# Kernel optimization log

Hardware: AMD Instinct MI355X
Metric: run time of the kernel (lower is better)

Reference implementation:

```python
import jax, jax.numpy as jnp
import numpy as np

TOP_K = 8  # num_experts_per_tok


def setup_inputs() -> dict:
    key = jax.random.key(0)
    ks = jax.random.split(key, 5)
    B, S, H = 2, 2048, 1024
    E, F = 16, 2816
    return {
        "hidden_states": jax.random.normal(ks[0], (B, S, H), dtype=jnp.float32),
        "router_w": jax.random.normal(ks[1], (E, H), dtype=jnp.float32) * (1.0 / np.sqrt(H)),
        "gate_w": jax.random.normal(ks[2], (E, F, H), dtype=jnp.float32) * (1.0 / np.sqrt(H)),
        "up_w": jax.random.normal(ks[3], (E, F, H), dtype=jnp.float32) * (1.0 / np.sqrt(H)),
        "down_w": jax.random.normal(ks[4], (E, H, F), dtype=jnp.float32) * (1.0 / np.sqrt(F)),
    }


def reference(hidden_states, router_w, gate_w, up_w, down_w):
    B, S, H = hidden_states.shape
    E = router_w.shape[0]
    x = hidden_states.reshape(-1, H)            # [T, H]
    T = x.shape[0]

    # Router: top-k expert selection, softmax over selected logits.
    logits = x @ router_w.T                      # [T, E]
    topk_vals, topk_idx = jax.lax.top_k(logits, TOP_K)
    topk_w = jax.nn.softmax(topk_vals, axis=-1)  # [T, K], sums to 1 -> no renorm needed

    # Dense combine weights [T, E] (scatter top-k weights per token).
    dense_w = jnp.zeros((T, E), dtype=x.dtype).at[
        jnp.arange(T)[:, None], topk_idx
    ].add(topk_w)

    # SwiGLU expert MLPs, batched over all experts (dense MoE reference).
    g = jnp.einsum('th,efh->etf', x, gate_w)     # [E, T, F]
    u = jnp.einsum('th,efh->etf', x, up_w)       # [E, T, F]
    h = jax.nn.silu(g) * u                       # [E, T, F]
    out_e = jnp.einsum('etf,ehf->eth', h, down_w)  # [E, T, H]

    out = jnp.einsum('te,eth->th', dense_w, out_e)  # weighted combine
    return out.reshape(B, S, H)
```

## Files before the change

kernel.cpp:

```cpp
#include <hip/hip_runtime.h>
#include <hip/hip_bf16.h>
#include <stdint.h>
#include <math.h>

#define T_TOK 4096
#define HD    1024
#define NE    16
#define FF    2816
#define TOPK  8
#define NPAIR (T_TOK*TOPK)

typedef __attribute__((ext_vector_type(8))) __bf16 bf16x8;
typedef __attribute__((ext_vector_type(4))) float  f32x4;

__device__ __forceinline__ unsigned short f2bf(float x){
  union { float f; unsigned u; } c; c.f = x;
  unsigned r = (c.u + 0x7FFFu + ((c.u >> 16) & 1u)) >> 16;
  return (unsigned short)r;
}
__device__ __forceinline__ float bf2f(unsigned short h){
  union { unsigned u; float f; } c; c.u = ((unsigned)h) << 16; return c.f;
}

__device__ __forceinline__ void gload16(const void* src, void* lds_dst){
  __builtin_amdgcn_global_load_lds((const __attribute__((address_space(1))) unsigned int*)src,
                                   (__attribute__((address_space(3))) unsigned int*)lds_dst,
                                   16, 0, 0);
}

__global__ __launch_bounds__(256) void convert3_kernel(
    const float* __restrict__ g, const float* __restrict__ u, const float* __restrict__ d,
    unsigned short* __restrict__ gb, unsigned short* __restrict__ ub, unsigned short* __restrict__ db,
    int n4each)
{
  int i = blockIdx.x * blockDim.x + threadIdx.x;
  int stride = gridDim.x * blockDim.x;
  int total = 3 * n4each;
  for (; i < total; i += stride){
    const float* s; unsigned short* dst; int j;
    if (i < n4each){ s = g; dst = gb; j = i; }
    else if (i < 2*n4each){ s = u; dst = ub; j = i - n4each; }
    else { s = d; dst = db; j = i - 2*n4each; }
    float4 v = ((const float4*)s)[j];
    ushort4 o;
    o.x = f2bf(v.x); o.y = f2bf(v.y); o.z = f2bf(v.z); o.w = f2bf(v.w);
    ((ushort4*)dst)[j] = o;
  }
}

__global__ __launch_bounds__(256) void router_kernel(
    const float* __restrict__ x, const float* __restrict__ rw,
    unsigned short* __restrict__ xbf, int* __restrict__ topk_idx, float* __restrict__ topk_w)
{
  __shared__ float xs[HD];
  __shared__ float lg[NE];
  const int t   = blockIdx.x;
  const int tid = threadIdx.x;
  const int lane = tid & 63;
  const int wid  = tid >> 6;

  float4 v = ((const float4*)(x + (size_t)t*HD))[tid];
  ((float4*)xs)[tid] = v;
  ushort4 o;
  o.x = f2bf(v.x); o.y = f2bf(v.y); o.z = f2bf(v.z); o.w = f2bf(v.w);
  ((ushort4*)(xbf + (size_t)t*HD))[tid] = o;
  __syncthreads();

  for (int ee = 0; ee < 4; ++ee){
    int e = wid*4 + ee;
    const float* w = rw + (size_t)e*HD;
    float p = 0.f;
    for (int j = lane; j < HD; j += 64) p += xs[j] * w[j];
    #pragma unroll
    for (int offs = 32; offs; offs >>= 1) p += __shfl_xor(p, offs, 64);
    if (lane == 0) lg[e] = p;
  }
  __syncthreads();

  if (tid == 0){
    float vals[NE];
    #pragma unroll
    for (int e = 0; e < NE; ++e) vals[e] = lg[e];
    int   idx[TOPK]; float tv[TOPK];
    for (int k = 0; k < TOPK; ++k){
      int bi = 0; float bv = -3.4e38f;
      for (int e = 0; e < NE; ++e) if (vals[e] > bv){ bv = vals[e]; bi = e; }
      idx[k] = bi; tv[k] = bv; vals[bi] = -3.4e38f;
    }
    float m = tv[0];
    float ex[TOPK]; float s = 0.f;
    for (int k = 0; k < TOPK; ++k){ ex[k] = expf(tv[k] - m); s += ex[k]; }
    float inv = 1.f / s;
    for (int k = 0; k < TOPK; ++k){
      topk_idx[t*TOPK + k] = idx[k];
      topk_w [t*TOPK + k] = ex[k] * inv;
    }
  }
}

__global__ __launch_bounds__(256) void lists_kernel(
    const int* __restrict__ topk_idx,
    int* __restrict__ rows, int* __restrict__ slot_of,
    int* __restrict__ cnt, int* __restrict__ offs_out)
{
  const int e = blockIdx.x;
  const int tid = threadIdx.x;
  const int lane = tid & 63;
  const int wid  = tid >> 6;

  __shared__ int wred[4];
  __shared__ int wred2[4];
  __shared__ int soff;

  int nlt = 0, ceq = 0;
  for (int t = tid; t < T_TOK; t += 256){
    #pragma unroll
    for (int k = 0; k < TOPK; ++k){
      int vv = topk_idx[t*TOPK + k];
      nlt += (vv < e) ? 1 : 0;
      ceq += (vv == e) ? 1 : 0;
    }
  }
  #pragma unroll
  for (int offs = 32; offs; offs >>= 1){
    nlt += __shfl_xor(nlt, offs, 64);
    ceq += __shfl_xor(ceq, offs, 64);
  }
  if (lane == 0){ wred[wid] = nlt; wred2[wid] = ceq; }
  __syncthreads();
  if (tid == 0){
    int off = wred[0] + wred[1] + wred[2] + wred[3];
    int c   = wred2[0] + wred2[1] + wred2[2] + wred2[3];
    offs_out[e] = off;
    cnt[e] = c;
    soff = off;
  }
  __syncthreads();
  const int off = soff;

  __shared__ int wc[4];
  int base = 0;
  for (int c0 = 0; c0 < T_TOK; c0 += 256){
    int t = c0 + tid;
    int kpos = -1;
    #pragma unroll
    for (int k = 0; k < TOPK; ++k) if (topk_idx[t*TOPK + k] == e) kpos = k;
    bool f = (kpos >= 0);
    unsigned long long m = __ballot(f);
    if (lane == 0) wc[wid] = __popcll(m);
    __syncthreads();
    int p = base;
    for (int w = 0; w < wid; ++w) p += wc[w];
    p += __popcll(m & ((1ULL << lane) - 1ULL));
    if (f){
      rows[off + p] = t;
      slot_of[t*TOPK + kpos] = off + p;
    }
    int tot = wc[0] + wc[1] + wc[2] + wc[3];
    __syncthreads();
    base += tot;
  }
}

__global__ __launch_bounds__(256, 3) void gemm_gateup(
    const unsigned short* __restrict__ xbf,
    const unsigned short* __restrict__ gw,
    const unsigned short* __restrict__ uw,
    const int* __restrict__ rows, const int* __restrict__ cnt, const int* __restrict__ offs,
    unsigned short* __restrict__ hbuf)
{
  const int cpx = gridDim.x >> 3;
  const int bid = blockIdx.x;
  const int nid = (bid & 7) * cpx + (bid >> 3);
  const int mb   = nid & 31;
  const int rest = nid >> 5;
  const int nb   = rest % (FF/64);
  const int e    = rest / (FF/64);

  const int c  = cnt[e];
  const int m0 = mb * 128;
  if (m0 >= c) return;
  const int n0 = nb * 64;
  const int off_e = offs[e];

  __shared__ unsigned short As[128*64];
  __shared__ unsigned short Bg[64*64];
  __shared__ unsigned short Bu[64*64];

  const int tid  = threadIdx.x;
  const int lane = tid & 63;
  const int wid  = tid >> 6;
  const int ar = lane & 15;
  const int kb = lane >> 4;
  const int wm = wid >> 1;
  const int wn = wid & 1;

  const unsigned short* asrc[4];
  #pragma unroll
  for (int j = 0; j < 4; ++j){
    int cj = j*256 + tid;
    int r  = cj >> 3;
    int sw = ((cj & 7) ^ (r & 7)) * 8;
    int rm = m0 + r; if (rm > c-1) rm = c-1;
    asrc[j] = xbf + (size_t)rows[off_e + rm]*HD + sw;
  }
  const unsigned short* bgsrc[2];
  const unsigned short* busrc[2];
  #pragma unroll
  for (int j = 0; j < 2; ++j){
    int cj = j*256 + tid;
    int r  = cj >> 3;
    int sw = ((cj & 7) ^ (r & 7)) * 8;
    bgsrc[j] = gw + ((size_t)e*FF + n0 + r)*HD + sw;
    busrc[j] = uw + ((size_t)e*FF + n0 + r)*HD + sw;
  }

  f32x4 accg[4][2] = {};
  f32x4 accu[4][2] = {};

  for (int ks = 0; ks < HD/64; ++ks){
    #pragma unroll
    for (int j = 0; j < 4; ++j)
      gload16(asrc[j] + ks*64, &As[(j*256+tid)*8]);
    #pragma unroll
    for (int j = 0; j < 2; ++j){
      gload16(bgsrc[j] + ks*64, &Bg[(j*256+tid)*8]);
      gload16(busrc[j] + ks*64, &Bu[(j*256+tid)*8]);
    }
    __syncthreads();
    #pragma unroll
    for (int kk = 0; kk < 2; ++kk){
      bf16x8 a[4], fg[2], fu[2];
      #pragma unroll
      for (int m = 0; m < 4; ++m){
        int r = wm*64 + m*16 + ar;
        a[m] = *(const bf16x8*)&As[r*64 + (((kk*4 + kb) ^ (r & 7))*8)];
      }
      #pragma unroll
      for (int n = 0; n < 2; ++n){
        int rf = wn*32 + n*16 + ar;
        int o  = rf*64 + (((kk*4 + kb) ^ (rf & 7))*8);
        fg[n] = *(const bf16x8*)&Bg[o];
        fu[n] = *(const bf16x8*)&Bu[o];
      }
      #pragma unroll
      for (int m = 0; m < 4; ++m){
        #pragma unroll
        for (int n = 0; n < 2; ++n){
          accg[m][n] = __builtin_amdgcn_mfma_f32_16x16x32_bf16(a[m], fg[n], accg[m][n], 0, 0, 0);
          accu[m][n] = __builtin_amdgcn_mfma_f32_16x16x32_bf16(a[m], fu[n], accu[m][n], 0, 0, 0);
        }
      }
    }
    __syncthreads();
  }

  #pragma unroll
  for (int m = 0; m < 4; ++m){
    #pragma unroll
    for (int n = 0; n < 2; ++n){
      int fcol = n0 + wn*32 + n*16 + ar;
      #pragma unroll
      for (int i = 0; i < 4; ++i){
        int gr = m0 + wm*64 + m*16 + kb*4 + i;
        if (gr < c){
          float g = accg[m][n][i];
          float u = accu[m][n][i];
          float s = g / (1.0f + expf(-g));
          hbuf[(size_t)(off_e + gr)*FF + fcol] = f2bf(s * u);
        }
      }
    }
  }
}

__global__ __launch_bounds__(256, 3) void gemm_down(
    const unsigned short* __restrict__ hbuf,
    const unsigned short* __restrict__ dw,
    const int* __restrict__ cnt, const int* __restrict__ offs,
    unsigned short* __restrict__ ybuf)
{
  const int cpx = gridDim.x >> 3;
  const int bid = blockIdx.x;
  const int nid = (bid & 7) * cpx + (bid >> 3);
  const int mb   = nid & 31;
  const int rest = nid >> 5;
  const int nb   = rest & 7;
  const int e    = rest >> 3;

  const int c  = cnt[e];
  const int m0 = mb * 128;
  if (m0 >= c) return;
  const int n0 = nb * 128;
  const int off_e = offs[e];

  __shared__ unsigned short As[128*64];
  __shared__ unsigned short Bs[128*64];

  const int tid  = threadIdx.x;
  const int lane = tid & 63;
  const int wid  = tid >> 6;
  const int ar = lane & 15;
  const int kb = lane >> 4;
  const int wm = wid >> 1;
  const int wn = wid & 1;

  const unsigned short* asrc[4];
  const unsigned short* bsrc[4];
  #pragma unroll
  for (int j = 0; j < 4; ++j){
    int cj = j*256 + tid;
    int r  = cj >> 3;
    int sw = ((cj & 7) ^ (r & 7)) * 8;
    int rm = m0 + r; if (rm > c-1) rm = c-1;
    asrc[j] = hbuf + (size_t)(off_e + rm)*FF + sw;
    bsrc[j] = dw + ((size_t)e*HD + n0 + r)*FF + sw;
  }

  f32x4 acc[4][4] = {};

  for (int ks = 0; ks < FF/64; ++ks){
    #pragma unroll
    for (int j = 0; j < 4; ++j){
      gload16(asrc[j] + ks*64, &As[(j*256+tid)*8]);
      gload16(bsrc[j] + ks*64, &Bs[(j*256+tid)*8]);
    }
    __syncthreads();
    #pragma unroll
    for (int kk = 0; kk < 2; ++kk){
      bf16x8 a[4], b[4];
      #pragma unroll
      for (int m = 0; m < 4; ++m){
        int r = wm*64 + m*16 + ar;
        a[m] = *(const bf16x8*)&As[r*64 + (((kk*4 + kb) ^ (r & 7))*8)];
      }
      #pragma unroll
      for (int n = 0; n < 4; ++n){
        int r = wn*64 + n*16 + ar;
        b[n] = *(const bf16x8*)&Bs[r*64 + (((kk*4 + kb) ^ (r & 7))*8)];
      }
      #pragma unroll
      for (int m = 0; m < 4; ++m){
        #pragma unroll
        for (int n = 0; n < 4; ++n){
          acc[m][n] = __builtin_amdgcn_mfma_f32_16x16x32_bf16(a[m], b[n], acc[m][n], 0, 0, 0);
        }
      }
    }
    __syncthreads();
  }

  #pragma unroll
  for (int m = 0; m < 4; ++m){
    #pragma unroll
    for (int n = 0; n < 4; ++n){
      int col = n0 + wn*64 + n*16 + ar;
      #pragma unroll
      for (int i = 0; i < 4; ++i){
        int gr = m0 + wm*64 + m*16 + kb*4 + i;
        if (gr < c){
          ybuf[(size_t)(off_e + gr)*HD + col] = f2bf(acc[m][n][i]);
        }
      }
    }
  }
}

__global__ __launch_bounds__(256) void combine_kernel(
    const unsigned short* __restrict__ ybuf,
    const int* __restrict__ slot_of, const float* __restrict__ topk_w,
    float* __restrict__ out)
{
  const int t   = blockIdx.x;
  const int tid = threadIdx.x;
  const int c0  = tid * 4;
  float4 acc = {0.f, 0.f, 0.f, 0.f};
  #pragma unroll
  for (int k = 0; k < TOPK; ++k){
    int slot = slot_of[t*TOPK + k];
    float w  = topk_w[t*TOPK + k];
    ushort4 v = *(const ushort4*)&ybuf[(size_t)slot*HD + c0];
    acc.x += w * bf2f(v.x);
    acc.y += w * bf2f(v.y);
    acc.z += w * bf2f(v.z);
    acc.w += w * bf2f(v.w);
  }
  ((float4*)out)[(size_t)t*(HD/4) + tid] = acc;
}

extern "C" void kernel_launch(void* const* d_in, const int* in_sizes, int n_in,
                              void* d_out, int out_size, void* d_ws, size_t ws_size,
                              hipStream_t stream)
{
  const float* x  = (const float*)d_in[0];
  const float* rw = (const float*)d_in[1];
  const float* gw = (const float*)d_in[2];
  const float* uw = (const float*)d_in[3];
  const float* dw = (const float*)d_in[4];
  float* out = (float*)d_out;

  char* ws = (char*)d_ws;
  size_t off = 0;
  auto alloc = [&](size_t b) -> void* {
    void* p = ws + off;
    off += (b + 255) & ~(size_t)255;
    return p;
  };

  unsigned short* gwb  = (unsigned short*)alloc((size_t)NE*FF*HD*2);
  unsigned short* uwb  = (unsigned short*)alloc((size_t)NE*FF*HD*2);
  unsigned short* dwb  = (unsigned short*)alloc((size_t)NE*HD*FF*2);
  unsigned short* xbf  = (unsigned short*)alloc((size_t)T_TOK*HD*2);
  unsigned short* hbuf = (unsigned short*)alloc((size_t)NPAIR*FF*2);
  unsigned short* ybuf = (unsigned short*)alloc((size_t)NPAIR*HD*2);
  int*   tki   = (int*)alloc((size_t)T_TOK*TOPK*4);
  float* tkw   = (float*)alloc((size_t)T_TOK*TOPK*4);
  int*   rowsb = (int*)alloc((size_t)NPAIR*4);
  int*   slotf = (int*)alloc((size_t)NPAIR*4);
  int*   cntb  = (int*)alloc(NE*4);
  int*   offsb = (int*)alloc(NE*4);

  const int n4 = NE*FF*HD/4;
  convert3_kernel<<<4096, 256, 0, stream>>>(gw, uw, dw, gwb, uwb, dwb, n4);

  router_kernel<<<T_TOK, 256, 0, stream>>>(x, rw, xbf, tki, tkw);
  lists_kernel<<<NE, 256, 0, stream>>>(tki, rowsb, slotf, cntb, offsb);

  gemm_gateup<<<32*(FF/64)*NE, 256, 0, stream>>>(xbf, gwb, uwb, rowsb, cntb, offsb, hbuf);
  gemm_down<<<32*(HD/128)*NE, 256, 0, stream>>>(hbuf, dwb, cntb, offsb, ybuf);

  combine_kernel<<<T_TOK, 256, 0, stream>>>(ybuf, slotf, tkw, out);
}
```

Measured before the change: 860.1 us.

## Fuse fp32-to-bf16 weight conversion into GEMM tile loads, drop convert kernel

Removes the separate pass that converted all expert weights from fp32 to bf16 into workspace. Each GEMM now loads fp32 weight tiles directly into registers, converts them to bf16, and stores them into the swizzled LDS layout. This saves a full read and write of about 553MB of weights. In exchange, the weight tiles are read in fp32 (twice the bytes per GEMM load), and the same weights are re-read by many M-blocks per expert. Because the load-to-LDS path is replaced by register loads plus conversion, there is also less overlap.

```diff
diff --git a/kernel.cpp b/kernel.cpp
--- a/kernel.cpp
+++ b/kernel.cpp
@@ -12,6 +12,7 @@
 
 typedef __attribute__((ext_vector_type(8))) __bf16 bf16x8;
 typedef __attribute__((ext_vector_type(4))) float  f32x4;
+typedef __attribute__((ext_vector_type(8))) unsigned short u16x8;
 
 __device__ __forceinline__ unsigned short f2bf(float x){
   union { float f; unsigned u; } c; c.f = x;
@@ -21,31 +22,17 @@
 __device__ __forceinline__ float bf2f(unsigned short h){
   union { unsigned u; float f; } c; c.u = ((unsigned)h) << 16; return c.f;
 }
+__device__ __forceinline__ u16x8 pack8(float4 a, float4 b){
+  u16x8 p;
+  p[0]=f2bf(a.x); p[1]=f2bf(a.y); p[2]=f2bf(a.z); p[3]=f2bf(a.w);
+  p[4]=f2bf(b.x); p[5]=f2bf(b.y); p[6]=f2bf(b.z); p[7]=f2bf(b.w);
+  return p;
+}
 
 __device__ __forceinline__ void gload16(const void* src, void* lds_dst){
   __builtin_amdgcn_global_load_lds((const __attribute__((address_space(1))) unsigned int*)src,
                                    (__attribute__((address_space(3))) unsigned int*)lds_dst,
                                    16, 0, 0);
-}
-
-__global__ __launch_bounds__(256) void convert3_kernel(
-    const float* __restrict__ g, const float* __restrict__ u, const float* __restrict__ d,
-    unsigned short* __restrict__ gb, unsigned short* __restrict__ ub, unsigned short* __restrict__ db,
-    int n4each)
-{
-  int i = blockIdx.x * blockDim.x + threadIdx.x;
-  int stride = gridDim.x * blockDim.x;
-  int total = 3 * n4each;
-  for (; i < total; i += stride){
-    const float* s; unsigned short* dst; int j;
-    if (i < n4each){ s = g; dst = gb; j = i; }
-    else if (i < 2*n4each){ s = u; dst = ub; j = i - n4each; }
-    else { s = d; dst = db; j = i - 2*n4each; }
-    float4 v = ((const float4*)s)[j];
-    ushort4 o;
-    o.x = f2bf(v.x); o.y = f2bf(v.y); o.z = f2bf(v.z); o.w = f2bf(v.w);
-    ((ushort4*)dst)[j] = o;
-  }
 }
 
 __global__ __launch_bounds__(256) void router_kernel(
@@ -164,8 +151,8 @@
 
 __global__ __launch_bounds__(256, 3) void gemm_gateup(
     const unsigned short* __restrict__ xbf,
-    const unsigned short* __restrict__ gw,
-    const unsigned short* __restrict__ uw,
+    const float* __restrict__ gw,
+    const float* __restrict__ uw,
     const int* __restrict__ rows, const int* __restrict__ cnt, const int* __restrict__ offs,
     unsigned short* __restrict__ hbuf)
 {
@@ -204,29 +191,31 @@
     int rm = m0 + r; if (rm > c-1) rm = c-1;
     asrc[j] = xbf + (size_t)rows[off_e + rm]*HD + sw;
   }
-  const unsigned short* bgsrc[2];
-  const unsigned short* busrc[2];
-  #pragma unroll
-  for (int j = 0; j < 2; ++j){
-    int cj = j*256 + tid;
-    int r  = cj >> 3;
-    int sw = ((cj & 7) ^ (r & 7)) * 8;
-    bgsrc[j] = gw + ((size_t)e*FF + n0 + r)*HD + sw;
-    busrc[j] = uw + ((size_t)e*FF + n0 + r)*HD + sw;
-  }
+
+  const int br = tid >> 2;
+  const int bq = tid & 3;
+  const float* bgbase = gw + ((size_t)e*FF + n0 + br)*HD + bq*16;
+  const float* bubase = uw + ((size_t)e*FF + n0 + br)*HD + bq*16;
+  unsigned short* bgdst0 = &Bg[br*64 + (((bq*2    ) ^ (br & 7))*8)];
+  unsigned short* bgdst1 = &Bg[br*64 + (((bq*2 + 1) ^ (br & 7))*8)];
+  unsigned short* budst0 = &Bu[br*64 + (((bq*2    ) ^ (br & 7))*8)];
+  unsigned short* budst1 = &Bu[br*64 + (((bq*2 + 1) ^ (br & 7))*8)];
 
   f32x4 accg[4][2] = {};
   f32x4 accu[4][2] = {};
 
   for (int ks = 0; ks < HD/64; ++ks){
+    const float4* gp = (const float4*)(bgbase + ks*64);
+    const float4* up = (const float4*)(bubase + ks*64);
+    float4 g0 = gp[0], g1 = gp[1], g2 = gp[2], g3 = gp[3];
+    float4 u0 = up[0], u1 = up[1], u2 = up[2], u3 = up[3];
     #pragma unroll
     for (int j = 0; j < 4; ++j)
       gload16(asrc[j] + ks*64, &As[(j*256+tid)*8]);
-    #pragma unroll
-    for (int j = 0; j < 2; ++j){
-      gload16(bgsrc[j] + ks*64, &Bg[(j*256+tid)*8]);
-      gload16(busrc[j] + ks*64, &Bu[(j*256+tid)*8]);
-    }
+    *(u16x8*)bgdst0 = pack8(g0, g1);
+    *(u16x8*)bgdst1 = pack8(g2, g3);
+    *(u16x8*)budst0 = pack8(u0, u1);
+    *(u16x8*)budst1 = pack8(u2, u3);
     __syncthreads();
     #pragma unroll
     for (int kk = 0; kk < 2; ++kk){
@@ -276,7 +265,7 @@
 
 __global__ __launch_bounds__(256, 3) void gemm_down(
     const unsigned short* __restrict__ hbuf,
-    const unsigned short* __restrict__ dw,
+    const float* __restrict__ dw,
     const int* __restrict__ cnt, const int* __restrict__ offs,
     unsigned short* __restrict__ ybuf)
 {
@@ -306,7 +295,6 @@
   const int wn = wid & 1;
 
   const unsigned short* asrc[4];
-  const unsigned short* bsrc[4];
   #pragma unroll
   for (int j = 0; j < 4; ++j){
     int cj = j*256 + tid;
@@ -314,17 +302,29 @@
     int sw = ((cj & 7) ^ (r & 7)) * 8;
     int rm = m0 + r; if (rm > c-1) rm = c-1;
     asrc[j] = hbuf + (size_t)(off_e + rm)*FF + sw;
-    bsrc[j] = dw + ((size_t)e*HD + n0 + r)*FF + sw;
-  }
+  }
+
+  const int br = tid >> 1;
+  const int bq = tid & 1;
+  const float* bbase = dw + ((size_t)e*HD + n0 + br)*FF + bq*32;
+  unsigned short* bdst[4];
+  #pragma unroll
+  for (int j = 0; j < 4; ++j)
+    bdst[j] = &Bs[br*64 + (((bq*4 + j) ^ (br & 7))*8)];
 
   f32x4 acc[4][4] = {};
 
   for (int ks = 0; ks < FF/64; ++ks){
-    #pragma unroll
-    for (int j = 0; j < 4; ++j){
+    const float4* bp = (const float4*)(bbase + ks*64);
+    float4 b0 = bp[0], b1 = bp[1], b2 = bp[2], b3 = bp[3];
+    float4 b4 = bp[4], b5 = bp[5], b6 = bp[6], b7 = bp[7];
+    #pragma unroll
+    for (int j = 0; j < 4; ++j)
       gload16(asrc[j] + ks*64, &As[(j*256+tid)*8]);
-      gload16(bsrc[j] + ks*64, &Bs[(j*256+tid)*8]);
-    }
+    *(u16x8*)bdst[0] = pack8(b0, b1);
+    *(u16x8*)bdst[1] = pack8(b2, b3);
+    *(u16x8*)bdst[2] = pack8(b4, b5);
+    *(u16x8*)bdst[3] = pack8(b6, b7);
     __syncthreads();
     #pragma unroll
     for (int kk = 0; kk < 2; ++kk){
@@ -407,9 +407,6 @@
     return p;
   };
 
-  unsigned short* gwb  = (unsigned short*)alloc((size_t)NE*FF*HD*2);
-  unsigned short* uwb  = (unsigned short*)alloc((size_t)NE*FF*HD*2);
-  unsigned short* dwb  = (unsigned short*)alloc((size_t)NE*HD*FF*2);
   unsigned short* xbf  = (unsigned short*)alloc((size_t)T_TOK*HD*2);
   unsigned short* hbuf = (unsigned short*)alloc((size_t)NPAIR*FF*2);
   unsigned short* ybuf = (unsigned short*)alloc((size_t)NPAIR*HD*2);
@@ -420,14 +417,11 @@
   int*   cntb  = (int*)alloc(NE*4);
   int*   offsb = (int*)alloc(NE*4);
 
-  const int n4 = NE*FF*HD/4;
-  convert3_kernel<<<4096, 256, 0, stream>>>(gw, uw, dw, gwb, uwb, dwb, n4);
-
   router_kernel<<<T_TOK, 256, 0, stream>>>(x, rw, xbf, tki, tkw);
   lists_kernel<<<NE, 256, 0, stream>>>(tki, rowsb, slotf, cntb, offsb);
 
-  gemm_gateup<<<32*(FF/64)*NE, 256, 0, stream>>>(xbf, gwb, uwb, rowsb, cntb, offsb, hbuf);
-  gemm_down<<<32*(HD/128)*NE, 256, 0, stream>>>(hbuf, dwb, cntb, offsb, ybuf);
+  gemm_gateup<<<32*(FF/64)*NE, 256, 0, stream>>>(xbf, gw, uw, rowsb, cntb, offsb, hbuf);
+  gemm_down<<<32*(HD/128)*NE, 256, 0, stream>>>(hbuf, dw, cntb, offsb, ybuf);
 
   combine_kernel<<<T_TOK, 256, 0, stream>>>(ybuf, slotf, tkw, out);
 }
```

Result: slower. 1.523 ms (+77.1%).

## Overlap weight conversion with router and gate/up GEMM via block-specialized fused kernels

Applied to the files above, without the earlier changes.

Removes the standalone fp32-to-bf16 conversion kernel. Gate/up weight conversion now runs in the even blocks of a fused router kernel, alongside the odd router blocks. Down-projection weight conversion is handed to every 12th block of the gate/up GEMM grid, so it overlaps GEMM work before gemm_down needs it. The aim is to hide the bandwidth-bound conversion behind compute and cut launches. In exchange, converter blocks compete for bandwidth and slots with the GEMM and router blocks, and the block index remapping adds complexity.

```diff
diff --git a/kernel.cpp b/kernel.cpp
--- a/kernel.cpp
+++ b/kernel.cpp
@@ -28,34 +28,35 @@
                                    16, 0, 0);
 }
 
-__global__ __launch_bounds__(256) void convert3_kernel(
-    const float* __restrict__ g, const float* __restrict__ u, const float* __restrict__ d,
-    unsigned short* __restrict__ gb, unsigned short* __restrict__ ub, unsigned short* __restrict__ db,
-    int n4each)
-{
-  int i = blockIdx.x * blockDim.x + threadIdx.x;
-  int stride = gridDim.x * blockDim.x;
-  int total = 3 * n4each;
-  for (; i < total; i += stride){
-    const float* s; unsigned short* dst; int j;
-    if (i < n4each){ s = g; dst = gb; j = i; }
-    else if (i < 2*n4each){ s = u; dst = ub; j = i - n4each; }
-    else { s = d; dst = db; j = i - 2*n4each; }
-    float4 v = ((const float4*)s)[j];
-    ushort4 o;
-    o.x = f2bf(v.x); o.y = f2bf(v.y); o.z = f2bf(v.z); o.w = f2bf(v.w);
-    ((ushort4*)dst)[j] = o;
-  }
-}
-
-__global__ __launch_bounds__(256) void router_kernel(
+__global__ __launch_bounds__(256) void convgu_router_kernel(
+    const float* __restrict__ g, const float* __restrict__ u,
+    unsigned short* __restrict__ gb, unsigned short* __restrict__ ub,
     const float* __restrict__ x, const float* __restrict__ rw,
     unsigned short* __restrict__ xbf, int* __restrict__ topk_idx, float* __restrict__ topk_w)
 {
   __shared__ float xs[HD];
   __shared__ float lg[NE];
-  const int t   = blockIdx.x;
   const int tid = threadIdx.x;
+
+  if ((blockIdx.x & 1) == 0){
+    const int n4 = NE*FF*HD/4;
+    const int cid = blockIdx.x >> 1;
+    int i = cid*256 + tid;
+    const int stride = 4096*256;
+    const int total = 2*n4;
+    for (; i < total; i += stride){
+      const float* s; unsigned short* dst; int j;
+      if (i < n4){ s = g; dst = gb; j = i; }
+      else { s = u; dst = ub; j = i - n4; }
+      float4 v = ((const float4*)s)[j];
+      ushort4 o;
+      o.x = f2bf(v.x); o.y = f2bf(v.y); o.z = f2bf(v.z); o.w = f2bf(v.w);
+      ((ushort4*)dst)[j] = o;
+    }
+    return;
+  }
+
+  const int t   = blockIdx.x >> 1;
   const int lane = tid & 63;
   const int wid  = tid >> 6;
 
@@ -167,13 +168,30 @@
     const unsigned short* __restrict__ gw,
     const unsigned short* __restrict__ uw,
     const int* __restrict__ rows, const int* __restrict__ cnt, const int* __restrict__ offs,
-    unsigned short* __restrict__ hbuf)
+    unsigned short* __restrict__ hbuf,
+    const float* __restrict__ dwf, unsigned short* __restrict__ dwb)
 {
   const int cpx = gridDim.x >> 3;
   const int bid = blockIdx.x;
   const int nid = (bid & 7) * cpx + (bid >> 3);
-  const int mb   = nid & 31;
-  const int rest = nid >> 5;
+  const int q  = nid / 12;
+  const int rr = nid - q*12;
+
+  if (rr == 11){
+    const int n4 = NE*HD*FF/4;
+    int i = q*256 + threadIdx.x;
+    const int stride = 2048*256;
+    for (; i < n4; i += stride){
+      float4 v = ((const float4*)dwf)[i];
+      ushort4 o;
+      o.x = f2bf(v.x); o.y = f2bf(v.y); o.z = f2bf(v.z); o.w = f2bf(v.w);
+      ((ushort4*)dwb)[i] = o;
+    }
+    return;
+  }
+  const int gid = q*11 + rr;
+  const int mb   = gid & 31;
+  const int rest = gid >> 5;
   const int nb   = rest % (FF/64);
   const int e    = rest / (FF/64);
 
@@ -420,13 +438,12 @@
   int*   cntb  = (int*)alloc(NE*4);
   int*   offsb = (int*)alloc(NE*4);
 
-  const int n4 = NE*FF*HD/4;
-  convert3_kernel<<<4096, 256, 0, stream>>>(gw, uw, dw, gwb, uwb, dwb, n4);
-
-  router_kernel<<<T_TOK, 256, 0, stream>>>(x, rw, xbf, tki, tkw);
+  convgu_router_kernel<<<8192, 256, 0, stream>>>(gw, uw, gwb, uwb,
+                                                 x, rw, xbf, tki, tkw);
   lists_kernel<<<NE, 256, 0, stream>>>(tki, rowsb, slotf, cntb, offsb);
 
-  gemm_gateup<<<32*(FF/64)*NE, 256, 0, stream>>>(xbf, gwb, uwb, rowsb, cntb, offsb, hbuf);
+  gemm_gateup<<<32*(FF/64)*NE + 2048, 256, 0, stream>>>(
+      xbf, gwb, uwb, rowsb, cntb, offsb, hbuf, dw, dwb);
   gemm_down<<<32*(HD/128)*NE, 256, 0, stream>>>(hbuf, dwb, cntb, offsb, ybuf);
 
   combine_kernel<<<T_TOK, 256, 0, stream>>>(ybuf, slotf, tkw, out);
```

Measured after the change: 824.4 us. -4.2%, faster.
